# Kernel optimization log

Measured on AMD Instinct MI355X. Metric: run time of the kernel, lower is better.

## Reference

```python
import jax, jax.numpy as jnp
import numpy as np

N_WIRES = 4


def _apply_rx(state, theta, wire):
    """Apply RX(theta) on `wire`. state: [B] + [2]*n complex; theta: [B] or scalar.
    RX(t) = cos(t/2) I - i sin(t/2) X, and X flips the wire axis."""
    n = state.ndim - 1
    half = theta * 0.5
    c = jnp.cos(half).astype(jnp.complex64)
    s = jnp.sin(half).astype(jnp.complex64)
    c = jnp.reshape(c, jnp.shape(c) + (1,) * n)
    s = jnp.reshape(s, jnp.shape(s) + (1,) * n)
    return c * state - 1j * s * jnp.flip(state, axis=wire + 1)


def _apply_cnot(state, control, target):
    """CNOT: flip target axis on the control=1 slice."""
    s0 = jax.lax.index_in_dim(state, 0, axis=control + 1, keepdims=True)
    s1 = jax.lax.index_in_dim(state, 1, axis=control + 1, keepdims=True)
    s1 = jnp.flip(s1, axis=target + 1)
    return jnp.concatenate([s0, s1], axis=control + 1)


def _encode(data, theta):
    """data: [B, n_wires] float angles -> [B, 2**n_wires] complex state."""
    B = data.shape[0]
    state = jnp.zeros((B,) + (2,) * N_WIRES, dtype=jnp.complex64)
    state = state.at[(slice(None),) + (0,) * N_WIRES].set(1.0)  # |0...0>
    for w in range(N_WIRES):              # data encoding RX per wire
        state = _apply_rx(state, data[:, w], w)
    for w in range(N_WIRES):              # trainable RX per wire
        state = _apply_rx(state, theta[w], w)
    for w in range(N_WIRES - 1):          # CNOT ladder
        state = _apply_cnot(state, w, w + 1)
    return state.reshape(B, 2 ** N_WIRES)


def setup_inputs() -> dict:
    key = jax.random.key(0)
    kx, ky, kt = jax.random.split(key, 3)
    x = jax.random.normal(kx, (8192, 4), dtype=jnp.float32)
    y = jax.random.normal(ky, (8192, 4), dtype=jnp.float32)
    theta = jax.random.normal(kt, (4,), dtype=jnp.float32)
    return {"x": x, "y": y, "theta": theta}


def reference(x, y, theta):
    states_x = _encode(x, theta)  # [Bx, 16] complex64
    states_y = _encode(y, theta)  # [By, 16] complex64
    # Faithful to torch source: plain matmul (no conjugate), then abs.
    return jnp.abs(states_x @ states_y.T)  # [Bx, By] float32
```

## Files before the change

kernel.cpp:

```cpp
#include <hip/hip_runtime.h>
#include <math.h>


#define BM 16
#define BN 256

__global__ __launch_bounds__(256) void qk_main(
    const float* __restrict__ x, const float* __restrict__ y,
    const float* __restrict__ theta, float* __restrict__ out,
    int Bx, int By)
{
    __shared__ float at[8][BM];
    __shared__ float bt[8][BN];

    const int tid = threadIdx.x;
    const int i0 = blockIdx.y * BM;
    const int j0 = blockIdx.x * BN;

    const float th0 = 0.5f * theta[0];
    const float th1 = 0.5f * theta[1];
    const float th2 = 0.5f * theta[2];
    const float th3 = 0.5f * theta[3];

    {
        const float4 y4 = ((const float4*)y)[j0 + tid];
        float s, c;
        __sincosf(0.5f * y4.x + th0, &s, &c); bt[0][tid] = c; bt[4][tid] = s;
        __sincosf(0.5f * y4.y + th1, &s, &c); bt[1][tid] = c; bt[5][tid] = s;
        __sincosf(0.5f * y4.z + th2, &s, &c); bt[2][tid] = c; bt[6][tid] = s;
        __sincosf(0.5f * y4.w + th3, &s, &c); bt[3][tid] = c; bt[7][tid] = s;
    }
    if (tid < BM) {
        const float4 x4 = ((const float4*)x)[i0 + tid];
        float s, c;
        __sincosf(0.5f * x4.x + th0, &s, &c); at[0][tid] = c; at[4][tid] = s;
        __sincosf(0.5f * x4.y + th1, &s, &c); at[1][tid] = c; at[5][tid] = s;
        __sincosf(0.5f * x4.z + th2, &s, &c); at[2][tid] = c; at[6][tid] = s;
        __sincosf(0.5f * x4.w + th3, &s, &c); at[3][tid] = c; at[7][tid] = s;
    }
    __syncthreads();

    const int tx = tid & 63;
    const int ty = tid >> 6;

    float acc[4][4];
    #pragma unroll
    for (int w = 0; w < 4; ++w) {
        const float4 ca = ((const float4*)&at[w][0])[ty];
        const float4 sa = ((const float4*)&at[w + 4][0])[ty];
        const float4 cb = ((const float4*)&bt[w][0])[tx];
        const float4 sb = ((const float4*)&bt[w + 4][0])[tx];

        const float cai[4] = {ca.x, ca.y, ca.z, ca.w};
        const float sai[4] = {sa.x, sa.y, sa.z, sa.w};
        const float cbj[4] = {cb.x, cb.y, cb.z, cb.w};
        const float sbj[4] = {sb.x, sb.y, sb.z, sb.w};

        #pragma unroll
        for (int i = 0; i < 4; ++i) {
            #pragma unroll
            for (int j = 0; j < 4; ++j) {
                const float t = fmaf(cai[i], cbj[j], -(sai[i] * sbj[j]));
                acc[i][j] = (w == 0) ? t : acc[i][j] * t;
            }
        }
    }

    #pragma unroll
    for (int i = 0; i < 4; ++i) {
        const int row = i0 + ty * 4 + i;
        float4 o;
        o.x = fabsf(acc[i][0]);
        o.y = fabsf(acc[i][1]);
        o.z = fabsf(acc[i][2]);
        o.w = fabsf(acc[i][3]);
        ((float4*)&out[(size_t)row * By + j0])[tx] = o;
    }
}

extern "C" void kernel_launch(void* const* d_in, const int* in_sizes, int n_in,
                              void* d_out, int out_size, void* d_ws, size_t ws_size,
                              hipStream_t stream) {
    const float* x     = (const float*)d_in[0];
    const float* y     = (const float*)d_in[1];
    const float* theta = (const float*)d_in[2];
    float* out = (float*)d_out;

    const int Bx = in_sizes[0] / 4;
    const int By = in_sizes[1] / 4;

    dim3 grid(By / BN, Bx / BM);
    qk_main<<<grid, dim3(256), 0, stream>>>(x, y, theta, out, Bx, By);
}
```

Baseline: 251.6 us.

## Stream multiple column tiles per block with register-resident trig factors

Adds a kernel where each block covers eight 256-column tiles and keeps each thread's row cos/sin factors in registers, so it drops shared memory and the block-wide barrier. Each thread now computes sincos for its own four y rows directly instead of sharing them through LDS. The goal is to amortize per-block setup and the x-side trig across more output, with fewer blocks and no synchronization. The cost is redundant y sincos across the four row groups of threads and higher register pressure. The old kernel remains as a fallback for sizes that don't divide evenly.

```diff
diff --git a/kernel.cpp b/kernel.cpp
--- a/kernel.cpp
+++ b/kernel.cpp
@@ -4,8 +4,70 @@
 
 #define BM 16
 #define BN 256
+#define TJ 8
 
-__global__ __launch_bounds__(256) void qk_main(
+__global__ __launch_bounds__(256) void qk_stream(
+    const float* __restrict__ x, const float* __restrict__ y,
+    const float* __restrict__ theta, float* __restrict__ out,
+    int Nx, int Ny)
+{
+    const int tid = threadIdx.x;
+    const int tx = tid & 63;
+    const int ty = tid >> 6;
+    const int i0 = blockIdx.y * BM;
+    const int j0 = blockIdx.x * (BN * TJ);
+    const int r0 = i0 + ty * 4;
+
+    const float th0 = 0.5f * theta[0], th1 = 0.5f * theta[1];
+    const float th2 = 0.5f * theta[2], th3 = 0.5f * theta[3];
+
+    float ca[4][4], sa[4][4];
+    #pragma unroll
+    for (int i = 0; i < 4; ++i) {
+        const float4 x4 = ((const float4*)x)[r0 + i];
+        __sincosf(0.5f * x4.x + th0, &sa[0][i], &ca[0][i]);
+        __sincosf(0.5f * x4.y + th1, &sa[1][i], &ca[1][i]);
+        __sincosf(0.5f * x4.z + th2, &sa[2][i], &ca[2][i]);
+        __sincosf(0.5f * x4.w + th3, &sa[3][i], &ca[3][i]);
+    }
+
+    #pragma unroll 2
+    for (int t = 0; t < TJ; ++t) {
+        const int j = j0 + t * BN + tx * 4;
+
+        float cb[4][4], sb[4][4];
+        #pragma unroll
+        for (int jj = 0; jj < 4; ++jj) {
+            const float4 y4 = ((const float4*)y)[j + jj];
+            __sincosf(0.5f * y4.x + th0, &sb[0][jj], &cb[0][jj]);
+            __sincosf(0.5f * y4.y + th1, &sb[1][jj], &cb[1][jj]);
+            __sincosf(0.5f * y4.z + th2, &sb[2][jj], &cb[2][jj]);
+            __sincosf(0.5f * y4.w + th3, &sb[3][jj], &cb[3][jj]);
+        }
+
+        float acc[4][4];
+        #pragma unroll
+        for (int i = 0; i < 4; ++i) {
+            #pragma unroll
+            for (int jj = 0; jj < 4; ++jj) {
+                const float t0 = fmaf(ca[0][i], cb[0][jj], -(sa[0][i] * sb[0][jj]));
+                const float t1 = fmaf(ca[1][i], cb[1][jj], -(sa[1][i] * sb[1][jj]));
+                const float t2 = fmaf(ca[2][i], cb[2][jj], -(sa[2][i] * sb[2][jj]));
+                const float t3 = fmaf(ca[3][i], cb[3][jj], -(sa[3][i] * sb[3][jj]));
+                acc[i][jj] = fabsf((t0 * t1) * (t2 * t3));
+            }
+        }
+
+        #pragma unroll
+        for (int i = 0; i < 4; ++i) {
+            float4 o;
+            o.x = acc[i][0]; o.y = acc[i][1]; o.z = acc[i][2]; o.w = acc[i][3];
+            *(float4*)&out[(size_t)(r0 + i) * Ny + j] = o;
+        }
+    }
+}
+
+__global__ __launch_bounds__(256) void qk_fallback(
     const float* __restrict__ x, const float* __restrict__ y,
     const float* __restrict__ theta, float* __restrict__ out,
     int Bx, int By)
@@ -81,6 +143,7 @@
 extern "C" void kernel_launch(void* const* d_in, const int* in_sizes, int n_in,
                               void* d_out, int out_size, void* d_ws, size_t ws_size,
                               hipStream_t stream) {
+    (void)n_in; (void)out_size; (void)d_ws; (void)ws_size;
     const float* x     = (const float*)d_in[0];
     const float* y     = (const float*)d_in[1];
     const float* theta = (const float*)d_in[2];
@@ -89,6 +152,11 @@
     const int Bx = in_sizes[0] / 4;
     const int By = in_sizes[1] / 4;
 
-    dim3 grid(By / BN, Bx / BM);
-    qk_main<<<grid, dim3(256), 0, stream>>>(x, y, theta, out, Bx, By);
+    if ((By % (BN * TJ)) == 0 && (Bx % BM) == 0) {
+        dim3 grid(By / (BN * TJ), Bx / BM);
+        qk_stream<<<grid, dim3(256), 0, stream>>>(x, y, theta, out, Bx, By);
+    } else {
+        dim3 grid(By / BN, Bx / BM);
+        qk_fallback<<<grid, dim3(256), 0, stream>>>(x, y, theta, out, Bx, By);
+    }
 }
```

New measurement: 259.0 us. +3.0%, slower.
